# Optimization experiments

Hardware: AMD Instinct MI355X
Metric: run time of the kernel (lower is better)

## Reference

```python
import jax, jax.numpy as jnp
import numpy as np
import math

B, N, D_IN, D_OUT, H = 8, 1024, 512, 512, 8
DH = D_OUT // H  # 64
SCALE = math.sqrt(DH)

def setup_inputs() -> dict:
    key = jax.random.key(0)
    ks = jax.random.split(key, 10)
    s_in = 1.0 / math.sqrt(D_IN)
    s_out = 1.0 / math.sqrt(D_OUT)
    return {
        "x": jax.random.normal(ks[0], (B, N, D_IN), dtype=jnp.float32),
        "Wq": jax.random.uniform(ks[1], (D_IN, D_OUT), jnp.float32, -s_in, s_in),
        "bq": jnp.zeros((D_OUT,), jnp.float32),
        "Wk": jax.random.uniform(ks[2], (D_IN, D_OUT), jnp.float32, -s_in, s_in),
        "bk": jnp.zeros((D_OUT,), jnp.float32),
        "Wv": jax.random.uniform(ks[3], (D_IN, D_OUT), jnp.float32, -s_in, s_in),
        "bv": jnp.zeros((D_OUT,), jnp.float32),
        "Wo": jax.random.uniform(ks[4], (D_OUT, D_OUT), jnp.float32, -s_out, s_out),
        "bo": jnp.zeros((D_OUT,), jnp.float32),
        # external distance-based positional bias buffer (num_heads, N, N)
        "pos_bias": 0.01 * jax.random.normal(ks[5], (H, N, N), dtype=jnp.float32),
    }

def reference(x, Wq, bq, Wk, bk, Wv, bv, Wo, bo, pos_bias):
    Bx, Nx, _ = x.shape
    # QKV projections -> (B, H, N, DH)
    def split_heads(t):
        return t.reshape(Bx, Nx, H, DH).transpose(0, 2, 1, 3)
    q = split_heads(x @ Wq + bq)
    k = split_heads(x @ Wk + bk)
    v = split_heads(x @ Wv + bv)
    # scaled dot-product scores with additive positional bias
    scores = jnp.einsum('bhnd,bhmd->bhnm', q, k) / SCALE + pos_bias[None]
    attn = jax.nn.softmax(scores, axis=-1)  # dropout p=0 (eval)
    out = jnp.einsum('bhnm,bhmd->bhnd', attn, v)
    out = out.transpose(0, 2, 1, 3).reshape(Bx, Nx, D_OUT)  # concat heads
    return out @ Wo + bo
```

## Files before the change

### kernel.cpp

```cpp
#include <hip/hip_runtime.h>
#include <hip/hip_bf16.h>
#include <stdint.h>


typedef __attribute__((ext_vector_type(4))) float f32x4;
typedef __attribute__((ext_vector_type(8))) short s16x8;
typedef __attribute__((ext_vector_type(4))) unsigned short u16x4;
typedef __attribute__((ext_vector_type(8))) unsigned short u16x8;

union FragAB { s16x8 v; u16x4 h[2]; unsigned u[4]; };

#define LOG2E 1.44269504089f
#define QSCALE (0.125f * LOG2E)

__device__ __forceinline__ unsigned short f2b(float f) {
  unsigned u = __builtin_bit_cast(unsigned, f);
  u = (u + 0x7FFFu + ((u >> 16) & 1u)) >> 16;
  return (unsigned short)u;
}
__device__ __forceinline__ unsigned cvt_pk(float a, float b) {
  unsigned r;
  asm("v_cvt_pk_bf16_f32 %0, %1, %2" : "=v"(r) : "v"(a), "v"(b));
  return r;
}
__device__ __forceinline__ void gl_lds16(const unsigned short* g, unsigned short* l) {
  __builtin_amdgcn_global_load_lds(
      (const __attribute__((address_space(1))) unsigned int*)(g),
      (__attribute__((address_space(3))) unsigned int*)(l), 16, 0, 0);
}

__global__ __launch_bounds__(256) void prep_k(const float* __restrict__ x,
                                              unsigned short* __restrict__ xb,
                                              const float* __restrict__ W0,
                                              const float* __restrict__ W1,
                                              const float* __restrict__ W2,
                                              const float* __restrict__ W3,
                                              unsigned short* __restrict__ Wt) {
  __shared__ float ld[64][68];
  const int t = threadIdx.x;
  if (blockIdx.x < 4096) {
    int idx = blockIdx.x * 256 + t;
    f32x4 v = ((const f32x4*)x)[idx];
    u16x4 o;
#pragma unroll
    for (int j = 0; j < 4; j++) o[j] = f2b(v[j]);
    ((u16x4*)xb)[idx] = o;
    return;
  }
  const int bid2 = blockIdx.x - 4096;
  const int widx = bid2 >> 6;
  const int tile = bid2 & 63;
  const int trow = tile >> 3, tcol = tile & 7;
  const float* W = widx == 0 ? W0 : widx == 1 ? W1 : widx == 2 ? W2 : W3;
  const int r = t >> 2, cc = (t & 3) * 16;
  const float* src = W + (size_t)(trow * 64 + r) * 512 + tcol * 64 + cc;
#pragma unroll
  for (int u = 0; u < 4; u++)
    ((f32x4*)&ld[r][cc])[u] = ((const f32x4*)src)[u];
  __syncthreads();
  unsigned short* dst = Wt + ((size_t)widx << 18) + (size_t)(tcol * 64 + r) * 512 +
                        trow * 64 + cc;
#pragma unroll
  for (int u = 0; u < 4; u++) {
    u16x4 o;
#pragma unroll
    for (int e = 0; e < 4; e++) o[e] = f2b(ld[cc + u * 4 + e][r]);
    ((u16x4*)dst)[u] = o;
  }
}

__global__ __launch_bounds__(256, 2) void gemm_qkv_k(const unsigned short* __restrict__ A,
                                                     const unsigned short* __restrict__ Bt,
                                                     const float* __restrict__ bq,
                                                     const float* __restrict__ bk,
                                                     const float* __restrict__ bv,
                                                     unsigned short* __restrict__ outp) {
  __shared__ unsigned short SM[2][2][128][32];
  const int tid = threadIdx.x;
  const int lane = tid & 63;
  const int w = tid >> 6;
  const int wm = w >> 1, wn = w & 1;
  const int g = lane >> 4, c = lane & 15;
  const int bn0 = (blockIdx.x % 12) * 128;
  const int bm0 = (blockIdx.x / 12) * 128;

  f32x4 acc[4][4];
#pragma unroll
  for (int i = 0; i < 4; i++)
#pragma unroll
    for (int j = 0; j < 4; j++) acc[i][j] = f32x4{0.f, 0.f, 0.f, 0.f};

  auto stage = [&](int buf, int kt) {
#pragma unroll
    for (int j = 0; j < 2; j++) {
      const int qb = (j * 4 + w) * 64;
      const int chunk = qb + lane;
      const int row = chunk >> 2, slot = chunk & 3;
      gl_lds16(A + (size_t)(bm0 + row) * 512 + kt * 32 + slot * 8,
               &SM[buf][0][0][0] + qb * 8);
      gl_lds16(Bt + (size_t)(bn0 + row) * 512 + kt * 32 + slot * 8,
               &SM[buf][1][0][0] + qb * 8);
    }
  };

  stage(0, 0);
  asm volatile("s_waitcnt vmcnt(0)" ::: "memory");
  __syncthreads();

  for (int kt = 0; kt < 16; ++kt) {
    const int cb = kt & 1;
    if (kt < 15) stage(cb ^ 1, kt + 1);

    FragAB af[4], bf[4];
#pragma unroll
    for (int mi = 0; mi < 4; mi++) {
      const u16x4* p = (const u16x4*)&SM[cb][0][wm * 64 + mi * 16 + c][g * 8];
      af[mi].h[0] = p[0]; af[mi].h[1] = p[1];
    }
#pragma unroll
    for (int ni = 0; ni < 4; ni++) {
      const u16x4* p = (const u16x4*)&SM[cb][1][wn * 64 + ni * 16 + c][g * 8];
      bf[ni].h[0] = p[0]; bf[ni].h[1] = p[1];
    }
    __builtin_amdgcn_s_setprio(1);
#pragma unroll
    for (int mi = 0; mi < 4; mi++)
#pragma unroll
      for (int ni = 0; ni < 4; ni++)
        acc[mi][ni] = __builtin_amdgcn_mfma_f32_16x16x32_bf16(af[mi].v, bf[ni].v,
                                                              acc[mi][ni], 0, 0, 0);
    __builtin_amdgcn_s_setprio(0);

    if (kt < 15) {
      asm volatile("s_waitcnt vmcnt(0)" ::: "memory");
      __syncthreads();
    }
  }

  __syncthreads();

  const int qkv = (bn0 + wn * 64) >> 9;
  const float* bp = qkv == 0 ? bq : (qkv == 1 ? bk : bv);
  const float scale = qkv == 0 ? QSCALE : 1.0f;
  const int b = (bm0 + wm * 64) >> 10;
  const int nb = (bm0 + wm * 64) & 1023;

  if (qkv == 2) {
    unsigned short* T = &SM[0][0][0][0] + w * 2176;
    const int hh = ((bn0 + wn * 64) & 511) >> 6;
    unsigned short* dst = outp + ((size_t)2 << 22) + ((size_t)((b << 3) + hh) << 16) + nb;
#pragma unroll
    for (int r2 = 0; r2 < 2; r2++) {
#pragma unroll
      for (int ni2 = 0; ni2 < 2; ni2++) {
        const int ni = r2 * 2 + ni2;
        const int dloc = ni2 * 16 + c;
        const float bvv = bp[(bn0 + wn * 64 + ni * 16 + c) & 511];
#pragma unroll
        for (int mi = 0; mi < 4; mi++) {
          const int n = mi * 16 + g * 4;
          *(unsigned*)&T[dloc * 68 + n] =
              cvt_pk(acc[mi][ni][0] + bvv, acc[mi][ni][1] + bvv);
          *(unsigned*)&T[dloc * 68 + n + 2] =
              cvt_pk(acc[mi][ni][2] + bvv, acc[mi][ni][3] + bvv);
        }
      }
      asm volatile("s_waitcnt lgkmcnt(0)" ::: "memory");
#pragma unroll
      for (int r = 0; r < 8; r++) {
        const int dloc = r * 4 + g;
        const u16x4 v4 = *(const u16x4*)&T[dloc * 68 + c * 4];
        *(u16x4*)(dst + ((size_t)(r2 * 32 + dloc) << 10) + c * 4) = v4;
      }
      if (r2 == 0) asm volatile("s_waitcnt lgkmcnt(0)" ::: "memory");
    }
  } else {
#pragma unroll
    for (int mi = 0; mi < 4; mi++)
#pragma unroll
      for (int ni = 0; ni < 4; ni++) {
        const int c9 = (bn0 + wn * 64 + ni * 16 + c) & 511;
        const float bvv = bp[c9];
        const int hh = c9 >> 6, d = c9 & 63;
#pragma unroll
        for (int m = 0; m < 4; m++) {
          const int n = nb + mi * 16 + g * 4 + m;
          const float v = (acc[mi][ni][m] + bvv) * scale;
          outp[((size_t)qkv << 22) + ((size_t)((b << 3) + hh) << 16) +
               ((size_t)n << 6) + d] = f2b(v);
        }
      }
  }
}

__global__ __launch_bounds__(512, 2) void gemm_o_k(const unsigned short* __restrict__ A,
                                                   const unsigned short* __restrict__ Bt,
                                                   const float* __restrict__ bias,
                                                   float* __restrict__ outp) {
  __shared__ unsigned short At[2][128][36];
  __shared__ unsigned short Bts[2][128][36];
  const int tid = threadIdx.x;
  const int lane = tid & 63;
  const int w = tid >> 6;
  const int wm = w >> 1, wn = w & 1;
  const int g = lane >> 4, c = lane & 15;
  const int bn0 = (blockIdx.x & 3) * 128;
  const int bm0 = (blockIdx.x >> 2) * 128;
  const int srow = tid >> 2;
  const int scol = (tid & 3) * 8;

  f32x4 acc[2][4];
#pragma unroll
  for (int i = 0; i < 2; i++)
#pragma unroll
    for (int j = 0; j < 4; j++) acc[i][j] = f32x4{0.f, 0.f, 0.f, 0.f};

  u16x8 ra, rb;
  auto ld = [&](int kt) {
    ra = *(const u16x8*)(A + (size_t)(bm0 + srow) * 512 + kt * 32 + scol);
    rb = *(const u16x8*)(Bt + (size_t)(bn0 + srow) * 512 + kt * 32 + scol);
  };
  auto st = [&](int b) {
    *(u16x8*)&At[b][srow][scol] = ra;
    *(u16x8*)&Bts[b][srow][scol] = rb;
  };

  ld(0); st(0);
  __syncthreads();

  for (int kt = 0; kt < 16; ++kt) {
    const int cb = kt & 1;
    if (kt < 15) ld(kt + 1);

    FragAB af[2], bf[4];
#pragma unroll
    for (int mi = 0; mi < 2; mi++) {
      const u16x4* p = (const u16x4*)&At[cb][wm * 32 + mi * 16 + c][g * 8];
      af[mi].h[0] = p[0]; af[mi].h[1] = p[1];
    }
#pragma unroll
    for (int ni = 0; ni < 4; ni++) {
      const u16x4* p = (const u16x4*)&Bts[cb][wn * 64 + ni * 16 + c][g * 8];
      bf[ni].h[0] = p[0]; bf[ni].h[1] = p[1];
    }
    __builtin_amdgcn_s_setprio(1);
#pragma unroll
    for (int mi = 0; mi < 2; mi++)
#pragma unroll
      for (int ni = 0; ni < 4; ni++)
        acc[mi][ni] = __builtin_amdgcn_mfma_f32_16x16x32_bf16(af[mi].v, bf[ni].v,
                                                              acc[mi][ni], 0, 0, 0);
    __builtin_amdgcn_s_setprio(0);

    if (kt < 15) {
      st(cb ^ 1);
      __syncthreads();
    }
  }

#pragma unroll
  for (int mi = 0; mi < 2; mi++) {
#pragma unroll
    for (int ni = 0; ni < 4; ni++) {
      const int col = bn0 + wn * 64 + ni * 16 + c;
      const float bv = bias[col];
#pragma unroll
      for (int m = 0; m < 4; m++) {
        const int row = bm0 + wm * 32 + mi * 16 + g * 4 + m;
        outp[(size_t)row * 512 + col] = acc[mi][ni][m] + bv;
      }
    }
  }
}

__global__ __launch_bounds__(256, 2) void attn_k(const unsigned short* __restrict__ Qb,
                                                 const unsigned short* __restrict__ Kb,
                                                 const unsigned short* __restrict__ Vt,
                                                 const float* __restrict__ pos_bias,
                                                 unsigned short* __restrict__ ao) {
  __shared__ unsigned short Klds[2][64][68];
  __shared__ unsigned short Vtlds[2][64][68];
  __shared__ unsigned short Plds[4][32][68];

  const int tid = threadIdx.x;
  const int lane = tid & 63;
  const int w = tid >> 6;
  const int g = lane >> 4, c = lane & 15;
  const int L = blockIdx.x;
  const int qt = L >> 6;
  const int bh = (L & 7) + 8 * ((L >> 3) & 7);
  const int h = bh & 7;
  const size_t bhq = (size_t)bh << 16;
  const int q0 = qt * 128 + w * 32;

  FragAB aq[2][2];
#pragma unroll
  for (int mi = 0; mi < 2; mi++)
#pragma unroll
    for (int kk = 0; kk < 2; kk++) {
      const u16x4* p = (const u16x4*)(Qb + bhq + ((size_t)(q0 + mi * 16 + c) << 6) +
                                      kk * 32 + g * 8);
      aq[mi][kk].h[0] = p[0]; aq[mi][kk].h[1] = p[1];
    }

  f32x4 acco[2][4];
#pragma unroll
  for (int mi = 0; mi < 2; mi++)
#pragma unroll
    for (int nd = 0; nd < 4; nd++) acco[mi][nd] = f32x4{0.f, 0.f, 0.f, 0.f};
  float lsum[2] = {0.f, 0.f};

  const int srow = tid >> 2;
  const int scol = (tid & 3) * 16;
  const unsigned short* pK = Kb + bhq + ((size_t)srow << 6) + scol;
  const unsigned short* pV = Vt + bhq + ((size_t)srow << 10) + scol;

  u16x8 kr0, kr1, vr0, vr1;
  auto stageLoad = [&](int k0n) {
    const u16x8* a = (const u16x8*)(pK + ((size_t)k0n << 6));
    kr0 = a[0]; kr1 = a[1];
    const u16x8* bb = (const u16x8*)(pV + k0n);
    vr0 = bb[0]; vr1 = bb[1];
  };
  auto stageWrite = [&](int b) {
    *(u16x8*)&Klds[b][srow][scol] = kr0;
    *(u16x8*)&Klds[b][srow][scol + 8] = kr1;
    *(u16x8*)&Vtlds[b][srow][scol] = vr0;
    *(u16x8*)&Vtlds[b][srow][scol + 8] = vr1;
  };

  const float* pbB = pos_bias + ((size_t)h << 20) + ((size_t)(q0 + c) << 10) + 4 * g;

  stageLoad(0);
  stageWrite(0);
  __syncthreads();

  for (int kt = 0; kt < 16; ++kt) {
    const int buf = kt & 1;
    const int k0 = kt << 6;
    if (kt < 15) stageLoad(k0 + 64);

    f32x4 pb[2][4];
#pragma unroll
    for (int mi = 0; mi < 2; mi++)
#pragma unroll
      for (int ni = 0; ni < 4; ni++)
        pb[mi][ni] = *(const f32x4*)(pbB + (mi << 14) + k0 + 16 * ni);

    FragAB bk[4][2];
#pragma unroll
    for (int ni = 0; ni < 4; ni++)
#pragma unroll
      for (int kk = 0; kk < 2; kk++) {
        const u16x4* p = (const u16x4*)&Klds[buf][ni * 16 + c][kk * 32 + g * 8];
        bk[ni][kk].h[0] = p[0]; bk[ni][kk].h[1] = p[1];
      }
    f32x4 sT[2][4];
    __builtin_amdgcn_s_setprio(1);
#pragma unroll
    for (int mi = 0; mi < 2; mi++)
#pragma unroll
      for (int ni = 0; ni < 4; ni++) {
        f32x4 s = f32x4{0.f, 0.f, 0.f, 0.f};
        s = __builtin_amdgcn_mfma_f32_16x16x32_bf16(bk[ni][0].v, aq[mi][0].v, s, 0, 0, 0);
        s = __builtin_amdgcn_mfma_f32_16x16x32_bf16(bk[ni][1].v, aq[mi][1].v, s, 0, 0, 0);
        sT[mi][ni] = s;
      }
    __builtin_amdgcn_s_setprio(0);

    FragAB vb2[4][2];
#pragma unroll
    for (int nd = 0; nd < 4; nd++)
#pragma unroll
      for (int kc = 0; kc < 2; kc++) {
        const u16x4* p = (const u16x4*)&Vtlds[buf][nd * 16 + c][kc * 32 + g * 8];
        vb2[nd][kc].h[0] = p[0]; vb2[nd][kc].h[1] = p[1];
      }

#pragma unroll
    for (int mi = 0; mi < 2; mi++)
#pragma unroll
      for (int ni = 0; ni < 4; ni++) {
        const float p0 = __builtin_amdgcn_exp2f(fmaf(pb[mi][ni][0], LOG2E, sT[mi][ni][0]));
        const float p1 = __builtin_amdgcn_exp2f(fmaf(pb[mi][ni][1], LOG2E, sT[mi][ni][1]));
        const float p2 = __builtin_amdgcn_exp2f(fmaf(pb[mi][ni][2], LOG2E, sT[mi][ni][2]));
        const float p3 = __builtin_amdgcn_exp2f(fmaf(pb[mi][ni][3], LOG2E, sT[mi][ni][3]));
        lsum[mi] += (p0 + p1) + (p2 + p3);
        uint2 two;
        two.x = cvt_pk(p0, p1);
        two.y = cvt_pk(p2, p3);
        *(uint2*)&Plds[w][mi * 16 + c][16 * ni + 4 * g] = two;
      }

    asm volatile("s_waitcnt lgkmcnt(0)" ::: "memory");

    FragAB paf[2][2];
#pragma unroll
    for (int mi = 0; mi < 2; mi++)
#pragma unroll
      for (int kc = 0; kc < 2; kc++) {
        const u16x4* p = (const u16x4*)&Plds[w][mi * 16 + c][kc * 32 + g * 8];
        paf[mi][kc].h[0] = p[0]; paf[mi][kc].h[1] = p[1];
      }
    __builtin_amdgcn_s_setprio(1);
#pragma unroll
    for (int mi = 0; mi < 2; mi++)
#pragma unroll
      for (int nd = 0; nd < 4; nd++) {
        acco[mi][nd] = __builtin_amdgcn_mfma_f32_16x16x32_bf16(paf[mi][0].v, vb2[nd][0].v,
                                                               acco[mi][nd], 0, 0, 0);
        acco[mi][nd] = __builtin_amdgcn_mfma_f32_16x16x32_bf16(paf[mi][1].v, vb2[nd][1].v,
                                                               acco[mi][nd], 0, 0, 0);
      }
    __builtin_amdgcn_s_setprio(0);

    if (kt < 15) {
      stageWrite(buf ^ 1);
      __syncthreads();
    }
  }

  const int b = bh >> 3;
#pragma unroll
  for (int mi = 0; mi < 2; mi++) {
    float l = lsum[mi];
    l += __shfl_xor(l, 16);
    l += __shfl_xor(l, 32);
    const float inv_c = 1.f / l;
#pragma unroll
    for (int m = 0; m < 4; m++) {
      const float invm = __shfl(inv_c, g * 4 + m);
      const int n = q0 + mi * 16 + g * 4 + m;
#pragma unroll
      for (int nd = 0; nd < 4; nd++) {
        ao[((size_t)(b * 1024 + n) << 9) + h * 64 + nd * 16 + c] =
            f2b(acco[mi][nd][m] * invm);
      }
    }
  }
}

extern "C" void kernel_launch(void* const* d_in, const int* in_sizes, int n_in,
                              void* d_out, int out_size, void* d_ws, size_t ws_size,
                              hipStream_t stream) {
  (void)in_sizes; (void)n_in; (void)out_size; (void)ws_size;
  const float* x  = (const float*)d_in[0];
  const float* Wq = (const float*)d_in[1];
  const float* bq = (const float*)d_in[2];
  const float* Wk = (const float*)d_in[3];
  const float* bk = (const float*)d_in[4];
  const float* Wv = (const float*)d_in[5];
  const float* bv = (const float*)d_in[6];
  const float* Wo = (const float*)d_in[7];
  const float* bo = (const float*)d_in[8];
  const float* pbias = (const float*)d_in[9];

  char* p = (char*)d_ws;
  unsigned short* xb  = (unsigned short*)p; p += (size_t)8192 * 512 * 2;
  unsigned short* WT  = (unsigned short*)p; p += (size_t)4 * 512 * 512 * 2;
  unsigned short* Qb  = (unsigned short*)p; p += (size_t)3 * 64 * 1024 * 64 * 2;
  unsigned short* AO  = (unsigned short*)p;

  unsigned short* WoT = WT + (size_t)3 * 512 * 512;
  unsigned short* Kb  = Qb + (size_t)64 * 1024 * 64;
  unsigned short* Vb  = Kb + (size_t)64 * 1024 * 64;

  prep_k<<<4352, 256, 0, stream>>>(x, xb, Wq, Wk, Wv, Wo, WT);
  gemm_qkv_k<<<768, 256, 0, stream>>>(xb, WT, bq, bk, bv, Qb);
  attn_k<<<512, 256, 0, stream>>>(Qb, Kb, Vb, pbias, AO);
  gemm_o_k<<<256, 512, 0, stream>>>(AO, WoT, bo, (float*)d_out);
}
```

Measured before the change: 81.60 us.

## Use direct global-to-LDS loads in output GEMM and prefetch positional bias one tile ahead

The output-projection GEMM now stages A and B tiles with direct global-to-LDS loads (gl_lds16) into an unpadded shared buffer, replacing the register round trip and explicit LDS stores. It waits on vmcnt before each barrier. The attention kernel double-buffers the pos_bias register tiles, loading the next key tile's bias during the current iteration via a two-step unrolled loop body, so global load latency is hidden behind the MFMA work. The risks are higher register pressure from two bias buffers, and possible LDS bank conflicts now that the padding is removed from the GEMM tiles.

```diff
diff --git a/kernel.cpp b/kernel.cpp
--- a/kernel.cpp
+++ b/kernel.cpp
@@ -197,8 +197,7 @@
                                                    const unsigned short* __restrict__ Bt,
                                                    const float* __restrict__ bias,
                                                    float* __restrict__ outp) {
-  __shared__ unsigned short At[2][128][36];
-  __shared__ unsigned short Bts[2][128][36];
+  __shared__ unsigned short SM[2][2][128][32];
   const int tid = threadIdx.x;
   const int lane = tid & 63;
   const int w = tid >> 6;
@@ -206,8 +205,6 @@
   const int g = lane >> 4, c = lane & 15;
   const int bn0 = (blockIdx.x & 3) * 128;
   const int bm0 = (blockIdx.x >> 2) * 128;
-  const int srow = tid >> 2;
-  const int scol = (tid & 3) * 8;
 
   f32x4 acc[2][4];
 #pragma unroll
@@ -215,32 +212,33 @@
 #pragma unroll
     for (int j = 0; j < 4; j++) acc[i][j] = f32x4{0.f, 0.f, 0.f, 0.f};
 
-  u16x8 ra, rb;
-  auto ld = [&](int kt) {
-    ra = *(const u16x8*)(A + (size_t)(bm0 + srow) * 512 + kt * 32 + scol);
-    rb = *(const u16x8*)(Bt + (size_t)(bn0 + srow) * 512 + kt * 32 + scol);
+  auto stage = [&](int buf, int kt) {
+    const int qb = w * 64;
+    const int chunk = qb + lane;
+    const int row = chunk >> 2, slot = chunk & 3;
+    gl_lds16(A + (size_t)(bm0 + row) * 512 + kt * 32 + slot * 8,
+             &SM[buf][0][0][0] + qb * 8);
+    gl_lds16(Bt + (size_t)(bn0 + row) * 512 + kt * 32 + slot * 8,
+             &SM[buf][1][0][0] + qb * 8);
   };
-  auto st = [&](int b) {
-    *(u16x8*)&At[b][srow][scol] = ra;
-    *(u16x8*)&Bts[b][srow][scol] = rb;
-  };
-
-  ld(0); st(0);
+
+  stage(0, 0);
+  asm volatile("s_waitcnt vmcnt(0)" ::: "memory");
   __syncthreads();
 
   for (int kt = 0; kt < 16; ++kt) {
     const int cb = kt & 1;
-    if (kt < 15) ld(kt + 1);
+    if (kt < 15) stage(cb ^ 1, kt + 1);
 
     FragAB af[2], bf[4];
 #pragma unroll
     for (int mi = 0; mi < 2; mi++) {
-      const u16x4* p = (const u16x4*)&At[cb][wm * 32 + mi * 16 + c][g * 8];
+      const u16x4* p = (const u16x4*)&SM[cb][0][wm * 32 + mi * 16 + c][g * 8];
       af[mi].h[0] = p[0]; af[mi].h[1] = p[1];
     }
 #pragma unroll
     for (int ni = 0; ni < 4; ni++) {
-      const u16x4* p = (const u16x4*)&Bts[cb][wn * 64 + ni * 16 + c][g * 8];
+      const u16x4* p = (const u16x4*)&SM[cb][1][wn * 64 + ni * 16 + c][g * 8];
       bf[ni].h[0] = p[0]; bf[ni].h[1] = p[1];
     }
     __builtin_amdgcn_s_setprio(1);
@@ -253,7 +251,7 @@
     __builtin_amdgcn_s_setprio(0);
 
     if (kt < 15) {
-      st(cb ^ 1);
+      asm volatile("s_waitcnt vmcnt(0)" ::: "memory");
       __syncthreads();
     }
   }
@@ -331,21 +329,28 @@
 
   const float* pbB = pos_bias + ((size_t)h << 20) + ((size_t)(q0 + c) << 10) + 4 * g;
 
+  f32x4 pbA[2][4], pbC[2][4];
+#pragma unroll
+  for (int mi = 0; mi < 2; mi++)
+#pragma unroll
+    for (int ni = 0; ni < 4; ni++)
+      pbA[mi][ni] = *(const f32x4*)(pbB + (mi << 14) + 16 * ni);
+
   stageLoad(0);
   stageWrite(0);
   __syncthreads();
 
-  for (int kt = 0; kt < 16; ++kt) {
+  auto body = [&](int kt, f32x4 (&pbu)[2][4], f32x4 (&pbn)[2][4]) {
     const int buf = kt & 1;
     const int k0 = kt << 6;
-    if (kt < 15) stageLoad(k0 + 64);
-
-    f32x4 pb[2][4];
-#pragma unroll
-    for (int mi = 0; mi < 2; mi++)
-#pragma unroll
-      for (int ni = 0; ni < 4; ni++)
-        pb[mi][ni] = *(const f32x4*)(pbB + (mi << 14) + k0 + 16 * ni);
+    if (kt < 15) {
+      stageLoad(k0 + 64);
+#pragma unroll
+      for (int mi = 0; mi < 2; mi++)
+#pragma unroll
+        for (int ni = 0; ni < 4; ni++)
+          pbn[mi][ni] = *(const f32x4*)(pbB + (mi << 14) + k0 + 64 + 16 * ni);
+    }
 
     FragAB bk[4][2];
 #pragma unroll
@@ -381,10 +386,10 @@
     for (int mi = 0; mi < 2; mi++)
 #pragma unroll
       for (int ni = 0; ni < 4; ni++) {
-        const float p0 = __builtin_amdgcn_exp2f(fmaf(pb[mi][ni][0], LOG2E, sT[mi][ni][0]));
-        const float p1 = __builtin_amdgcn_exp2f(fmaf(pb[mi][ni][1], LOG2E, sT[mi][ni][1]));
-        const float p2 = __builtin_amdgcn_exp2f(fmaf(pb[mi][ni][2], LOG2E, sT[mi][ni][2]));
-        const float p3 = __builtin_amdgcn_exp2f(fmaf(pb[mi][ni][3], LOG2E, sT[mi][ni][3]));
+        const float p0 = __builtin_amdgcn_exp2f(fmaf(pbu[mi][ni][0], LOG2E, sT[mi][ni][0]));
+        const float p1 = __builtin_amdgcn_exp2f(fmaf(pbu[mi][ni][1], LOG2E, sT[mi][ni][1]));
+        const float p2 = __builtin_amdgcn_exp2f(fmaf(pbu[mi][ni][2], LOG2E, sT[mi][ni][2]));
+        const float p3 = __builtin_amdgcn_exp2f(fmaf(pbu[mi][ni][3], LOG2E, sT[mi][ni][3]));
         lsum[mi] += (p0 + p1) + (p2 + p3);
         uint2 two;
         two.x = cvt_pk(p0, p1);
@@ -418,6 +423,11 @@
       stageWrite(buf ^ 1);
       __syncthreads();
     }
+  };
+
+  for (int kt2 = 0; kt2 < 16; kt2 += 2) {
+    body(kt2, pbA, pbC);
+    body(kt2 + 1, pbC, pbA);
   }
 
   const int b = bh >> 3;
```

Measured after the change: 91.46 us. +12.1%, slower.
